# Performance work log

Hardware: AMD Instinct MI355X
Metric: run time of the kernel (lower is better)

Reference implementation:

```python
import jax, jax.numpy as jnp
import numpy as np


def setup_inputs() -> dict:
    key = jax.random.key(0)
    k1, k2, k3, k4 = jax.random.split(key, 4)
    B, C, T = 32, 512, 1024
    N, D = 64, 512
    scale = 1.0 / np.sqrt(C)
    x = jax.random.normal(k1, (B, C, T), dtype=jnp.float32)
    subjects = jax.random.randint(k2, (B,), 0, N, dtype=jnp.int64)
    weights = jax.random.normal(k3, (N, C, D), dtype=jnp.float32) * scale
    bias = jax.random.normal(k4, (N, D), dtype=jnp.float32) * scale
    return {"x": x, "subjects": subjects, "weights": weights, "bias": bias}


def reference(x, subjects, weights, bias):
    # gather mode: per-example projection matrix, then batched GEMM
    # x: (B, C, T); weights[subjects]: (B, C, D) -> out: (B, D, T)
    w = weights[subjects]                      # (B, C, D)
    out = jnp.einsum('bct,bcd->bdt', x, w)
    out = out + bias[subjects][:, :, None]     # (B, D, 1) broadcast over T
    return out
```

## Files before the change

### kernel.cpp

```cpp
#include <hip/hip_runtime.h>
#include <hip/hip_bf16.h>

#define B_N 32
#define C_K 512
#define T_N 1024
#define D_M 512

constexpr int BM = 128, BN = 128, BK = 32;
constexpr int SA = 36;
constexpr int KSTEPS = C_K / BK;

typedef __attribute__((ext_vector_type(4))) float  floatx4;
typedef __attribute__((ext_vector_type(4))) short  shortx4;
typedef __attribute__((ext_vector_type(8))) short  shortx8;
typedef __attribute__((ext_vector_type(2))) unsigned int uintx2;

__device__ __forceinline__ unsigned pk2(float a, float b) {
  __hip_bfloat162 h = __float22bfloat162_rn(make_float2(a, b));
  union { __hip_bfloat162 v; unsigned u; } c; c.v = h; return c.u;
}

__global__ __launch_bounds__(256, 3)
void subject_gemm(const float* __restrict__ x, const int* __restrict__ subjects,
                  const float* __restrict__ weights, const float* __restrict__ bias,
                  float* __restrict__ out)
{
  __shared__ short lds_a[2][BM * SA];
  __shared__ short lds_b[2][BN * SA];

  const int bid  = blockIdx.x;
  const int xcd  = bid & 7;
  const int s    = bid >> 3;
  const int b    = xcd * 4 + (s & 3);
  const int tile = s >> 2;
  const int tm = tile >> 3, tn = tile & 7;
  const int m0 = tm * BM, n0 = tn * BN;
  const int nb = subjects[b];

  const float* __restrict__ Wp = weights + (size_t)nb * C_K * D_M;
  const float* __restrict__ Xp = x + (size_t)b * C_K * T_N;

  const int tid  = threadIdx.x;
  const int lane = tid & 63;
  const int wave = tid >> 6;

  const bool isA = (wave < 2);
  const int  mg  = (wave & 1) * 16 + (lane & 15);
  const int  oct = lane >> 4;
  const float* gsrc = isA ? (Wp + (size_t)(8 * oct) * D_M + (m0 + 4 * mg))
                          : (Xp + (size_t)(8 * oct) * T_N + (n0 + 4 * mg));
  const int gs = isA ? D_M : T_N;
  short* const wbase = (isA ? &lds_a[0][0] : &lds_b[0][0]) + (4 * mg) * SA + 8 * oct;
  constexpr int BUFO = BM * SA;

  const int wm = (wave & 1) * 64, wn = (wave >> 1) * 64;
  const int l15 = lane & 15, q = lane >> 4;

  floatx4 acc[4][4] = {};
  floatx4 v[8];

  #pragma unroll
  for (int jj = 0; jj < 8; ++jj)
    v[jj] = *(const floatx4*)(gsrc + (size_t)jj * gs);
  gsrc += (size_t)BK * gs;
  #pragma unroll
  for (int r = 0; r < 4; ++r) {
    uintx2 lo = { pk2(v[0][r], v[1][r]), pk2(v[2][r], v[3][r]) };
    uintx2 hi = { pk2(v[4][r], v[5][r]), pk2(v[6][r], v[7][r]) };
    *(uintx2*)(wbase + r * SA)     = lo;
    *(uintx2*)(wbase + r * SA + 4) = hi;
  }

  for (int ks = 0; ks < KSTEPS; ++ks) {
    const int p = ks & 1;
    __syncthreads();

    if (ks + 1 < KSTEPS) {
      #pragma unroll
      for (int jj = 0; jj < 8; ++jj)
        v[jj] = *(const floatx4*)(gsrc + (size_t)jj * gs);
      gsrc += (size_t)BK * gs;
    }

    const short* pa = &lds_a[p][0] + (wm + l15) * SA + 8 * q;
    const short* pb = &lds_b[p][0] + (wn + l15) * SA + 8 * q;
    shortx8 af[4], bg[4];
    #pragma unroll
    for (int i = 0; i < 4; ++i) {
      shortx4 alo = *(const shortx4*)(pa + 16 * i * SA);
      shortx4 ahi = *(const shortx4*)(pa + 16 * i * SA + 4);
      shortx4 blo = *(const shortx4*)(pb + 16 * i * SA);
      shortx4 bhi = *(const shortx4*)(pb + 16 * i * SA + 4);
      af[i] = __builtin_shufflevector(alo, ahi, 0, 1, 2, 3, 4, 5, 6, 7);
      bg[i] = __builtin_shufflevector(blo, bhi, 0, 1, 2, 3, 4, 5, 6, 7);
    }
    #pragma unroll
    for (int i = 0; i < 4; ++i)
      #pragma unroll
      for (int j = 0; j < 4; ++j)
        acc[i][j] = __builtin_amdgcn_mfma_f32_16x16x32_bf16(af[i], bg[j], acc[i][j], 0, 0, 0);

    if (ks + 1 < KSTEPS) {
      short* wdst = wbase + (p ^ 1) * BUFO;
      #pragma unroll
      for (int r = 0; r < 4; ++r) {
        uintx2 lo = { pk2(v[0][r], v[1][r]), pk2(v[2][r], v[3][r]) };
        uintx2 hi = { pk2(v[4][r], v[5][r]), pk2(v[6][r], v[7][r]) };
        *(uintx2*)(wdst + r * SA)     = lo;
        *(uintx2*)(wdst + r * SA + 4) = hi;
      }
    }
  }

  float* __restrict__ O = out + (size_t)b * D_M * T_N;
  const float* __restrict__ bb = bias + (size_t)nb * D_M;
  #pragma unroll
  for (int i = 0; i < 4; ++i) {
    #pragma unroll
    for (int r = 0; r < 4; ++r) {
      const int d = m0 + wm + 16 * i + 4 * q + r;
      const float bv = bb[d];
      #pragma unroll
      for (int j = 0; j < 4; ++j) {
        const int t = n0 + wn + 16 * j + l15;
        O[(size_t)d * T_N + t] = acc[i][j][r] + bv;
      }
    }
  }
}

extern "C" void kernel_launch(void* const* d_in, const int* in_sizes, int n_in,
                              void* d_out, int out_size, void* d_ws, size_t ws_size,
                              hipStream_t stream) {
  const float* x        = (const float*)d_in[0];
  const int*   subjects = (const int*)d_in[1];
  const float* weights  = (const float*)d_in[2];
  const float* bias     = (const float*)d_in[3];
  float* out = (float*)d_out;
  (void)in_sizes; (void)n_in; (void)out_size; (void)d_ws; (void)ws_size;

  dim3 grid(B_N * 4 * 8);
  dim3 block(256);
  hipLaunchKernelGGL(subject_gemm, grid, block, 0, stream, x, subjects, weights, bias, out);
}
```

Measured before the change: 181.5 us.

## Use 512-thread blocks with swizzled LDS and two-deep register prefetch pipeline

Doubles the workgroup to 8 waves, so each wave computes a 64x32 sub-tile and stages a quarter of the K-slab instead of half. Global loads are prefetched two K-steps ahead into alternating register sets, with a manually unrolled loop and a lightweight barrier. An XOR swizzle is added to the LDS write and read offsets to reduce bank conflicts. The aims are more latency hiding and higher occupancy, at the cost of more barrier participants, higher register pressure per thread, and more complex index arithmetic.

New measurement: 189.8 us. 4.6% more time.

```diff
diff --git a/kernel.cpp b/kernel.cpp
--- a/kernel.cpp
+++ b/kernel.cpp
@@ -9,6 +9,7 @@
 constexpr int BM = 128, BN = 128, BK = 32;
 constexpr int SA = 36;
 constexpr int KSTEPS = C_K / BK;
+constexpr int BUFO = BM * SA;
 
 typedef __attribute__((ext_vector_type(4))) float  floatx4;
 typedef __attribute__((ext_vector_type(4))) short  shortx4;
@@ -20,13 +21,19 @@
   union { __hip_bfloat162 v; unsigned u; } c; c.v = h; return c.u;
 }
 
-__global__ __launch_bounds__(256, 3)
+__device__ __forceinline__ void wg_barrier() {
+  asm volatile("s_waitcnt lgkmcnt(0)" ::: "memory");
+  __builtin_amdgcn_s_barrier();
+  __builtin_amdgcn_sched_barrier(0);
+}
+
+__global__ __launch_bounds__(512, 4)
 void subject_gemm(const float* __restrict__ x, const int* __restrict__ subjects,
                   const float* __restrict__ weights, const float* __restrict__ bias,
                   float* __restrict__ out)
 {
-  __shared__ short lds_a[2][BM * SA];
-  __shared__ short lds_b[2][BN * SA];
+  __shared__ __align__(16) short lds_a[2][BUFO];
+  __shared__ __align__(16) short lds_b[2][BUFO];
 
   const int bid  = blockIdx.x;
   const int xcd  = bid & 7;
@@ -44,73 +51,84 @@
   const int lane = tid & 63;
   const int wave = tid >> 6;
 
-  const bool isA = (wave < 2);
-  const int  mg  = (wave & 1) * 16 + (lane & 15);
-  const int  oct = lane >> 4;
-  const float* gsrc = isA ? (Wp + (size_t)(8 * oct) * D_M + (m0 + 4 * mg))
-                          : (Xp + (size_t)(8 * oct) * T_N + (n0 + 4 * mg));
+  const bool isA = (wave < 4);
+  const int  wv  = wave & 3;
+  const int  o   = lane >> 5;
+  const int  mg  = lane & 31;
+  const int  kq  = 2 * wv + o;
+  const float* gsrc = isA ? (Wp + (size_t)(4 * kq) * D_M + (m0 + 4 * mg))
+                          : (Xp + (size_t)(4 * kq) * T_N + (n0 + 4 * mg));
   const int gs = isA ? D_M : T_N;
-  short* const wbase = (isA ? &lds_a[0][0] : &lds_b[0][0]) + (4 * mg) * SA + 8 * oct;
-  constexpr int BUFO = BM * SA;
+  const int swz = (mg >> 2) & 3;
+  short* const wbase = (isA ? &lds_a[0][0] : &lds_b[0][0])
+                       + (4 * mg) * SA + 4 * (kq ^ swz);
 
-  const int wm = (wave & 1) * 64, wn = (wave >> 1) * 64;
+  const int wm = (wave & 1) * 64, wn = (wave >> 1) * 32;
+  const int w1 = (wave >> 1) & 1;
   const int l15 = lane & 15, q = lane >> 4;
 
-  floatx4 acc[4][4] = {};
-  floatx4 v[8];
+  floatx4 acc[4][2] = {};
+  floatx4 vA[4], vB[4];
 
-  #pragma unroll
-  for (int jj = 0; jj < 8; ++jj)
-    v[jj] = *(const floatx4*)(gsrc + (size_t)jj * gs);
-  gsrc += (size_t)BK * gs;
-  #pragma unroll
-  for (int r = 0; r < 4; ++r) {
-    uintx2 lo = { pk2(v[0][r], v[1][r]), pk2(v[2][r], v[3][r]) };
-    uintx2 hi = { pk2(v[4][r], v[5][r]), pk2(v[6][r], v[7][r]) };
-    *(uintx2*)(wbase + r * SA)     = lo;
-    *(uintx2*)(wbase + r * SA + 4) = hi;
-  }
-
-  for (int ks = 0; ks < KSTEPS; ++ks) {
-    const int p = ks & 1;
-    __syncthreads();
-
-    if (ks + 1 < KSTEPS) {
-      #pragma unroll
-      for (int jj = 0; jj < 8; ++jj)
-        v[jj] = *(const floatx4*)(gsrc + (size_t)jj * gs);
-      gsrc += (size_t)BK * gs;
+  auto loads = [&](floatx4 (&v)[4]) {
+    #pragma unroll
+    for (int jj = 0; jj < 4; ++jj)
+      v[jj] = *(const floatx4*)(gsrc + (size_t)jj * gs);
+    gsrc += (size_t)BK * gs;
+  };
+  auto cvt_store = [&](const floatx4 (&v)[4], int p) {
+    short* wdst = wbase + p * BUFO;
+    #pragma unroll
+    for (int r = 0; r < 4; ++r) {
+      uintx2 pk = { pk2(v[0][r], v[1][r]), pk2(v[2][r], v[3][r]) };
+      *(uintx2*)(wdst + r * SA) = pk;
     }
-
-    const short* pa = &lds_a[p][0] + (wm + l15) * SA + 8 * q;
-    const short* pb = &lds_b[p][0] + (wn + l15) * SA + 8 * q;
-    shortx8 af[4], bg[4];
+  };
+  auto compute = [&](int p) {
+    const short* pa = &lds_a[p][0] + (wm + l15) * SA;
+    const short* pb = &lds_b[p][0] + (wn + l15) * SA;
+    shortx8 af[4], bg[2];
     #pragma unroll
     for (int i = 0; i < 4; ++i) {
-      shortx4 alo = *(const shortx4*)(pa + 16 * i * SA);
-      shortx4 ahi = *(const shortx4*)(pa + 16 * i * SA + 4);
-      shortx4 blo = *(const shortx4*)(pb + 16 * i * SA);
-      shortx4 bhi = *(const shortx4*)(pb + 16 * i * SA + 4);
+      const int base = 16 * i * SA + 8 * (q ^ (i >> 1));
+      shortx4 alo = *(const shortx4*)(pa + base + 4 * (i & 1));
+      shortx4 ahi = *(const shortx4*)(pa + base + 4 * ((i & 1) ^ 1));
       af[i] = __builtin_shufflevector(alo, ahi, 0, 1, 2, 3, 4, 5, 6, 7);
-      bg[i] = __builtin_shufflevector(blo, bhi, 0, 1, 2, 3, 4, 5, 6, 7);
+    }
+    #pragma unroll
+    for (int j = 0; j < 2; ++j) {
+      const int base = 16 * j * SA + 8 * (q ^ w1);
+      shortx4 blo = *(const shortx4*)(pb + base + 4 * j);
+      shortx4 bhi = *(const shortx4*)(pb + base + 4 * (j ^ 1));
+      bg[j] = __builtin_shufflevector(blo, bhi, 0, 1, 2, 3, 4, 5, 6, 7);
     }
     #pragma unroll
     for (int i = 0; i < 4; ++i)
       #pragma unroll
-      for (int j = 0; j < 4; ++j)
+      for (int j = 0; j < 2; ++j)
         acc[i][j] = __builtin_amdgcn_mfma_f32_16x16x32_bf16(af[i], bg[j], acc[i][j], 0, 0, 0);
+  };
 
-    if (ks + 1 < KSTEPS) {
-      short* wdst = wbase + (p ^ 1) * BUFO;
-      #pragma unroll
-      for (int r = 0; r < 4; ++r) {
-        uintx2 lo = { pk2(v[0][r], v[1][r]), pk2(v[2][r], v[3][r]) };
-        uintx2 hi = { pk2(v[4][r], v[5][r]), pk2(v[6][r], v[7][r]) };
-        *(uintx2*)(wdst + r * SA)     = lo;
-        *(uintx2*)(wdst + r * SA + 4) = hi;
-      }
-    }
+  loads(vA);
+  loads(vB);
+  cvt_store(vA, 0);
+
+  #pragma unroll 1
+  for (int kk = 0; kk < KSTEPS - 2; kk += 2) {
+    wg_barrier();
+    loads(vA);
+    compute(0);
+    cvt_store(vB, 1);
+    wg_barrier();
+    loads(vB);
+    compute(1);
+    cvt_store(vA, 0);
   }
+  wg_barrier();
+  compute(0);
+  cvt_store(vB, 1);
+  wg_barrier();
+  compute(1);
 
   float* __restrict__ O = out + (size_t)b * D_M * T_N;
   const float* __restrict__ bb = bias + (size_t)nb * D_M;
@@ -121,7 +139,7 @@
       const int d = m0 + wm + 16 * i + 4 * q + r;
       const float bv = bb[d];
       #pragma unroll
-      for (int j = 0; j < 4; ++j) {
+      for (int j = 0; j < 2; ++j) {
         const int t = n0 + wn + 16 * j + l15;
         O[(size_t)d * T_N + t] = acc[i][j][r] + bv;
       }
@@ -140,6 +158,6 @@
   (void)in_sizes; (void)n_in; (void)out_size; (void)d_ws; (void)ws_size;
 
   dim3 grid(B_N * 4 * 8);
-  dim3 block(256);
+  dim3 block(512);
   hipLaunchKernelGGL(subject_gemm, grid, block, 0, stream, x, subjects, weights, bias, out);
 }
```
